# Kernel optimization log

Hardware: AMD Instinct MI355X
Metric: run time of the kernel (lower is better)

Reference implementation:

```python
import jax, jax.numpy as jnp
import numpy as np

H = 16
BN_EPS = 1e-12

def setup_inputs() -> dict:
    key = jax.random.key(0)
    ks = jax.random.split(key, 12)
    B, S, D = 2, 2048, 1024
    sc_in = 1.0 / np.sqrt(D)
    inp = {
        "hidden_states": jax.random.normal(ks[0], (B, S, D), jnp.float32),
        "attention_mask": jnp.zeros((B, 1, 1, S), jnp.float32),
        "Wq": jax.random.normal(ks[1], (D, D), jnp.float32) * sc_in,
        "bq": jnp.zeros((D,), jnp.float32),
        "Wk": jax.random.normal(ks[2], (D, D), jnp.float32) * sc_in,
        "bk": jnp.zeros((D,), jnp.float32),
        "Wv": jax.random.normal(ks[3], (D, D), jnp.float32) * sc_in,
        "bv": jnp.zeros((D,), jnp.float32),
        "pW1": jax.random.normal(ks[4], (D, 64), jnp.float32) * sc_in,
        "pb1": jnp.zeros((64,), jnp.float32),
        "bn_gamma": jnp.ones((64,), jnp.float32),
        "bn_beta": jnp.zeros((64,), jnp.float32),
        "bn_mean": jnp.zeros((64,), jnp.float32),
        "bn_var": jnp.ones((64,), jnp.float32),
        "pW2": jax.random.normal(ks[5], (64, H), jnp.float32) * (1.0 / 8.0),
        "pb2": jnp.zeros((H,), jnp.float32),
    }
    return inp


def reference(hidden_states, attention_mask, Wq, bq, Wk, bk, Wv, bv,
              pW1, pb1, bn_gamma, bn_beta, bn_mean, bn_var, pW2, pb2):
    B, S, D = hidden_states.shape
    hd = D // H
    scale = 1.0 / jnp.sqrt(jnp.asarray(hd, hidden_states.dtype))

    def split_heads(x):  # [B,S,D] -> [B,H,S,hd]
        return x.reshape(B, S, H, hd).transpose(0, 2, 1, 3)

    q = split_heads(hidden_states @ Wq + bq)
    k = split_heads(hidden_states @ Wk + bk)
    v = split_heads(hidden_states @ Wv + bv)

    scores = jnp.einsum("bhqd,bhkd->bhqk", q, k) * scale + attention_mask
    probs = jax.nn.softmax(scores, axis=-1)

    # head-gate predictor (layer_id == 0 -> mean pooling over sequence)
    pooled = jnp.mean(hidden_states, axis=1)  # [B,D]
    h = pooled @ pW1 + pb1
    h = (h - bn_mean) * jax.lax.rsqrt(bn_var + BN_EPS) * bn_gamma + bn_beta
    h = jax.nn.relu(h)
    logits = h @ pW2 + pb2  # [B,H]
    # inference-mode gumbel gate: hard threshold at 0
    head_gate = (logits >= 0).astype(probs.dtype)  # [B,H]

    probs = probs * head_gate[:, :, None, None]
    ctx = jnp.einsum("bhqk,bhkd->bhqd", probs, v)
    return ctx.transpose(0, 2, 1, 3).reshape(B, S, D)
```

## Files before the change

### kernel.cpp

```cpp
#include <hip/hip_runtime.h>

#define S_LEN 2048
#define D_DIM 1024
#define NH 16
#define HD 64
#define BATCH 2

#define QK_SCALE 0.18033688011112042f
#define LOG2E 1.4426950408889634f

using s16x8 = __attribute__((ext_vector_type(8))) short;
using u16x8 = __attribute__((ext_vector_type(8))) unsigned short;
using f32x4 = __attribute__((ext_vector_type(4))) float;
using bf16x8v = __attribute__((ext_vector_type(8))) __bf16;

typedef const __attribute__((address_space(1))) unsigned int* gas_ptr;
typedef __attribute__((address_space(3))) unsigned int* las_ptr;

__device__ __forceinline__ unsigned short f32_to_bf16(float f) {
  unsigned int u = __float_as_uint(f);
  u += 0x7FFFu + ((u >> 16) & 1u);
  return (unsigned short)(u >> 16);
}

__device__ __forceinline__ f32x4 mfma_bf16(s16x8 a, s16x8 b, f32x4 c) {
  return __builtin_amdgcn_mfma_f32_16x16x32_bf16(
      __builtin_bit_cast(bf16x8v, a), __builtin_bit_cast(bf16x8v, b), c, 0, 0, 0);
}

__device__ __forceinline__ float exp2_fast(float x) {
  float r;
  asm("v_exp_f32 %0, %1" : "=v"(r) : "v"(x));
  return r;
}

__device__ __forceinline__ unsigned int cvt_pk_bf16(float a, float b) {
  unsigned int r;
  asm("v_cvt_pk_bf16_f32 %0, %1, %2" : "=v"(r) : "v"(a), "v"(b));
  return r;
}

__global__ __launch_bounds__(256) void pool_cvt(const float* __restrict__ hs,
                                                unsigned short* __restrict__ hsb,
                                                float* __restrict__ partial) {
  int bid = blockIdx.x;
  int b = bid & 1;
  int chunk = (bid >> 1) & 31;
  int dq = bid >> 6;
  int d = dq * 256 + threadIdx.x;
  const float* p = hs + ((size_t)b * S_LEN + chunk * 64) * D_DIM + d;
  unsigned short* o = hsb + ((size_t)b * S_LEN + chunk * 64) * D_DIM + d;
  float s = 0.f;
  for (int i = 0; i < 64; ++i) {
    float v = p[(size_t)i * D_DIM];
    s += v;
    o[(size_t)i * D_DIM] = f32_to_bf16(v);
  }
  partial[(size_t)(b * 32 + chunk) * D_DIM + d] = s;
}

__global__ __launch_bounds__(256) void transpose_w3(
    const float* __restrict__ Wq, const float* __restrict__ Wk,
    const float* __restrict__ Wv, unsigned short* __restrict__ WTq,
    unsigned short* __restrict__ WTk, unsigned short* __restrict__ WTv) {
  __shared__ float tile[32][33];
  int z = blockIdx.z;
  const float* W = (z == 0) ? Wq : (z == 1) ? Wk : Wv;
  unsigned short* WT = (z == 0) ? WTq : (z == 1) ? WTk : WTv;
  float scale = (z == 0) ? QK_SCALE : 1.0f;
  int tx = threadIdx.x & 31;
  int ty = threadIdx.x >> 5;
  int c0 = blockIdx.x * 32;
  int r0 = blockIdx.y * 32;
#pragma unroll
  for (int i = 0; i < 4; ++i)
    tile[ty + i * 8][tx] = W[(r0 + ty + i * 8) * D_DIM + c0 + tx];
  __syncthreads();
#pragma unroll
  for (int i = 0; i < 4; ++i)
    WT[(c0 + ty + i * 8) * D_DIM + r0 + tx] = f32_to_bf16(tile[tx][ty + i * 8] * scale);
}

__global__ __launch_bounds__(512) void gate_kernel(
    const float* __restrict__ partial, const float* __restrict__ pW1,
    const float* __restrict__ pb1, const float* __restrict__ gamma,
    const float* __restrict__ beta, const float* __restrict__ mean,
    const float* __restrict__ var, const float* __restrict__ pW2,
    const float* __restrict__ pb2, float* __restrict__ gate) {
  __shared__ float pooled[2 * D_DIM];
  __shared__ float hsh[2][64];
  int t = threadIdx.x;
  for (int idx = t; idx < 2 * D_DIM; idx += 512) {
    int b = idx >> 10, k = idx & 1023;
    float s = 0.f;
#pragma unroll
    for (int c = 0; c < 32; ++c) s += partial[(size_t)(b * 32 + c) * D_DIM + k];
    pooled[idx] = s * (1.0f / 2048.0f);
  }
  __syncthreads();
  int b = t >> 8, jj = (t >> 2) & 63, quarter = t & 3;
  float acc = 0.f;
  for (int k = quarter * 256; k < quarter * 256 + 256; ++k)
    acc += pooled[b * D_DIM + k] * pW1[k * 64 + jj];
  acc += __shfl_xor(acc, 1, 64);
  acc += __shfl_xor(acc, 2, 64);
  if (quarter == 0) {
    acc += pb1[jj];
    acc = (acc - mean[jj]) * rsqrtf(var[jj] + 1e-12f) * gamma[jj] + beta[jj];
    hsh[b][jj] = fmaxf(acc, 0.f);
  }
  __syncthreads();
  if (t < 32) {
    int bb = t >> 4, hh = t & 15;
    float lg = pb2[hh];
#pragma unroll
    for (int kk = 0; kk < 64; ++kk) lg += hsh[bb][kk] * pW2[kk * NH + hh];
    gate[bb * NH + hh] = (lg >= 0.f) ? 1.f : 0.f;
  }
}

__global__ __launch_bounds__(256) void proj_gemm3(
    const unsigned short* __restrict__ A, const unsigned short* __restrict__ BT,
    const float* __restrict__ bq, const float* __restrict__ bk,
    const float* __restrict__ bv, unsigned short* __restrict__ Qb,
    unsigned short* __restrict__ Kb, unsigned short* __restrict__ Vtb) {
  __shared__ __align__(16) unsigned short As[128 * 64];
  __shared__ __align__(16) unsigned short Bs[128 * 64];
  int idx = blockIdx.x;
  int xcd = idx & 7, j = idx >> 3;
  int xm = xcd * 4 + j / 24;
  int yn = j % 24;
  int m0 = xm * 128, n0 = yn * 128;
  int tid = threadIdx.x, wave = tid >> 6, lane = tid & 63;
  int l15 = lane & 15, lhi = lane >> 4;
  int wm = (wave >> 1) * 64, wn = (wave & 1) * 64;
  f32x4 acc[4][4] = {};

  const unsigned short* asrc[4];
  const unsigned short* bsrc[4];
  int ldst[4];
#pragma unroll
  for (int r4 = 0; r4 < 4; ++r4) {
    int o = tid * 16 + r4 * 4096;
    int row = o >> 7;
    int e = ((o & 127) ^ ((row & 7) << 4)) >> 1;
    asrc[r4] = A + (size_t)(m0 + row) * D_DIM + e;
    bsrc[r4] = BT + (size_t)(n0 + row) * D_DIM + e;
    ldst[r4] = o >> 1;
  }
  int rsw = (l15 & 7) << 4;

  for (int k0 = 0; k0 < D_DIM; k0 += 64) {
#pragma unroll
    for (int r4 = 0; r4 < 4; ++r4) {
      __builtin_amdgcn_global_load_lds((gas_ptr)(asrc[r4] + k0),
                                       (las_ptr)(As + ldst[r4]), 16, 0, 0);
      __builtin_amdgcn_global_load_lds((gas_ptr)(bsrc[r4] + k0),
                                       (las_ptr)(Bs + ldst[r4]), 16, 0, 0);
    }
    __syncthreads();
    __builtin_amdgcn_s_setprio(1);
#pragma unroll
    for (int ks = 0; ks < 2; ++ks) {
      s16x8 af[4], bf[4];
#pragma unroll
      for (int mi = 0; mi < 4; ++mi)
        af[mi] = *(const s16x8*)((const char*)As + (wm + mi * 16 + l15) * 128 +
                                 ((ks * 64 + lhi * 16) ^ rsw));
#pragma unroll
      for (int ni = 0; ni < 4; ++ni)
        bf[ni] = *(const s16x8*)((const char*)Bs + (wn + ni * 16 + l15) * 128 +
                                 ((ks * 64 + lhi * 16) ^ rsw));
#pragma unroll
      for (int mi = 0; mi < 4; ++mi)
#pragma unroll
        for (int ni = 0; ni < 4; ++ni)
          acc[mi][ni] = mfma_bf16(af[mi], bf[ni], acc[mi][ni]);
    }
    __builtin_amdgcn_s_setprio(0);
    __syncthreads();
  }

#pragma unroll
  for (int mi = 0; mi < 4; ++mi)
#pragma unroll
    for (int ni = 0; ni < 4; ++ni) {
      int row0 = m0 + wm + mi * 16 + lhi * 4;
      int col = n0 + wn + ni * 16 + l15;
      int seg = col >> 10, c = col & 1023;
      if (seg == 2) {
        float bvv = bv[c];
        int h = c >> 6, d = c & 63;
        int b = row0 >> 11, s = row0 & 2047;
        ushort4 pk;
        pk.x = f32_to_bf16(acc[mi][ni][0] + bvv);
        pk.y = f32_to_bf16(acc[mi][ni][1] + bvv);
        pk.z = f32_to_bf16(acc[mi][ni][2] + bvv);
        pk.w = f32_to_bf16(acc[mi][ni][3] + bvv);
        *(ushort4*)&Vtb[((size_t)(b * NH + h) * HD + d) * S_LEN + s] = pk;
      } else {
        float bb2 = (seg == 0) ? bq[c] * QK_SCALE : bk[c];
        unsigned short* dst = (seg == 0) ? Qb : Kb;
        int h = c >> 6, d = c & 63;
#pragma unroll
        for (int r = 0; r < 4; ++r) {
          int row = row0 + r;
          int b = row >> 11, s = row & 2047;
          dst[((size_t)(b * NH + h) * S_LEN + s) * HD + d] =
              f32_to_bf16(acc[mi][ni][r] + bb2);
        }
      }
    }
}

__global__ __launch_bounds__(128) void attn_kernel(
    const unsigned short* __restrict__ Q, const unsigned short* __restrict__ K,
    const unsigned short* __restrict__ Vt, const float* __restrict__ mask,
    const float* __restrict__ gate, float* __restrict__ Out) {
  __shared__ __align__(16) unsigned short Ks[2][4096];
  __shared__ __align__(16) unsigned short Vs[2][4096];
  __shared__ __align__(16) unsigned short p_lds[2][2][1024];

  int idx = blockIdx.x;
  int xcd = idx & 7;
  int slot = idx >> 3;
  int qc = slot & 31;
  int r = (slot >> 5) * 8 + xcd;
  int tid = threadIdx.x;
  int wave = tid >> 6, lane = tid & 63;
  int l15 = lane & 15, lhi = lane >> 4;

  float gv = (lane < 32) ? gate[lane] : 0.f;
  unsigned long long live = __ballot(gv != 0.f);
  int W = __popcll(live);
  bool working = (r < W);
  int want = working ? r : (r - W);
  unsigned long long M = working ? live : (~live & 0xFFFFFFFFull);
  int head = 0, c = 0;
#pragma unroll
  for (int hh = 0; hh < 32; ++hh) {
    if ((M >> hh) & 1) {
      if (c == want) head = hh;
      ++c;
    }
  }
  int b = head >> 4, h = head & 15;

  if (!working) {
    float4 z = {0.f, 0.f, 0.f, 0.f};
    int row = qc * 64 + (tid >> 1);
    float* op = Out + ((size_t)b * S_LEN + row) * D_DIM + h * HD + (tid & 1) * 32;
#pragma unroll
    for (int dd = 0; dd < 8; ++dd) *(float4*)(op + dd * 4) = z;
    return;
  }

  int qA = qc * 64 + wave * 32 + l15;
  int qB = qA + 16;
  const unsigned short* Qp = Q + (size_t)head * S_LEN * HD;
  const unsigned short* Kp = K + (size_t)head * S_LEN * HD;
  const unsigned short* Vp = Vt + (size_t)head * HD * S_LEN;
  const float* maskp = mask + (size_t)b * S_LEN;

  int psw = (l15 & 7) << 4;
  const unsigned short* kb[4];
  const unsigned short* vb[4];
  int ldst[4];
#pragma unroll
  for (int j = 0; j < 4; ++j) {
    int o = tid * 16 + j * 2048;
    int row = o >> 7, col = o & 127;
    int e = (col ^ ((row & 7) << 4)) >> 1;
    kb[j] = Kp + row * HD + e;
    vb[j] = Vp + (size_t)row * S_LEN + e;
    ldst[j] = o >> 1;
  }

#define STAGE(BUFI, KTV)                                                           \
  {                                                                                \
    _Pragma("unroll") for (int j = 0; j < 4; ++j) {                                \
      __builtin_amdgcn_global_load_lds((gas_ptr)(kb[j] + (size_t)(KTV)*HD),        \
                                       (las_ptr)(&Ks[BUFI][ldst[j]]), 16, 0, 0);   \
      __builtin_amdgcn_global_load_lds((gas_ptr)(vb[j] + (KTV)),                   \
                                       (las_ptr)(&Vs[BUFI][ldst[j]]), 16, 0, 0);   \
    }                                                                              \
  }

  STAGE(0, 0);
  float4 mvc[4];
#pragma unroll
  for (int nf = 0; nf < 4; ++nf)
    mvc[nf] = *(const float4*)(maskp + nf * 16 + lhi * 4);

  s16x8 qfa[2], qfb[2];
#pragma unroll
  for (int ks = 0; ks < 2; ++ks) {
    qfa[ks] = *(const s16x8*)(Qp + (size_t)qA * HD + ks * 32 + lhi * 8);
    qfb[ks] = *(const s16x8*)(Qp + (size_t)qB * HD + ks * 32 + lhi * 8);
  }

  int swz0 = (lhi * 16) ^ psw;
  int swz1 = (64 + lhi * 16) ^ psw;
  char* pbaseA = (char*)p_lds + wave * 4096 + l15 * 128;
  char* pbaseB = pbaseA + 2048;

  f32x4 oa[4] = {}, ob[4] = {};
  float sa_run = 0.f, sb_run = 0.f;

  __syncthreads();

  for (int kt = 0; kt < S_LEN; kt += 64) {
    int buf = (kt >> 6) & 1;
    int ktn = (kt + 64) & (S_LEN - 1);
    STAGE(buf ^ 1, ktn);
    float4 mvn[4];
#pragma unroll
    for (int nf = 0; nf < 4; ++nf)
      mvn[nf] = *(const float4*)(maskp + ktn + nf * 16 + lhi * 4);

    const char* kc = (const char*)&Ks[0][0] + buf * 8192;
    f32x4 sa[4] = {}, sb[4] = {};
    __builtin_amdgcn_s_setprio(1);
#pragma unroll
    for (int nf = 0; nf < 4; ++nf) {
      int rb = (nf * 16 + l15) * 128;
      s16x8 a0 = *(const s16x8*)(kc + (rb + swz0));
      s16x8 a1 = *(const s16x8*)(kc + (rb + swz1));
      sa[nf] = mfma_bf16(a0, qfa[0], sa[nf]);
      sa[nf] = mfma_bf16(a1, qfa[1], sa[nf]);
      sb[nf] = mfma_bf16(a0, qfb[0], sb[nf]);
      sb[nf] = mfma_bf16(a1, qfb[1], sb[nf]);
    }
    __builtin_amdgcn_s_setprio(0);

    float psa[4], psb[4];
#pragma unroll
    for (int nf = 0; nf < 4; ++nf) {
#pragma unroll
      for (int rr = 0; rr < 4; ++rr) {
        float m2 = ((const float*)&mvc[nf])[rr] * LOG2E;
        sa[nf][rr] = exp2_fast(sa[nf][rr] + m2);
        sb[nf][rr] = exp2_fast(sb[nf][rr] + m2);
      }
      psa[nf] = (sa[nf][0] + sa[nf][1]) + (sa[nf][2] + sa[nf][3]);
      psb[nf] = (sb[nf][0] + sb[nf][1]) + (sb[nf][2] + sb[nf][3]);
    }
    sa_run += (psa[0] + psa[1]) + (psa[2] + psa[3]);
    sb_run += (psb[0] + psb[1]) + (psb[2] + psb[3]);

#pragma unroll
    for (int nf = 0; nf < 4; ++nf) {
      uint2 pka, pkb;
      pka.x = cvt_pk_bf16(sa[nf][0], sa[nf][1]);
      pka.y = cvt_pk_bf16(sa[nf][2], sa[nf][3]);
      pkb.x = cvt_pk_bf16(sb[nf][0], sb[nf][1]);
      pkb.y = cvt_pk_bf16(sb[nf][2], sb[nf][3]);
      int off = (nf * 32 + lhi * 8) ^ psw;
      *(uint2*)(pbaseA + off) = pka;
      *(uint2*)(pbaseB + off) = pkb;
    }

    const char* vc = (const char*)&Vs[0][0] + buf * 8192;
    __builtin_amdgcn_s_setprio(1);
#pragma unroll
    for (int ks = 0; ks < 2; ++ks) {
      int sw = ks ? swz1 : swz0;
      int poff = (ks * 64 + lhi * 16) ^ psw;
      s16x8 pfa = *(const s16x8*)(pbaseA + poff);
      s16x8 pfb = *(const s16x8*)(pbaseB + poff);
#pragma unroll
      for (int df = 0; df < 4; ++df) {
        s16x8 vf = *(const s16x8*)(vc + ((df * 16 + l15) * 128 + sw));
        oa[df] = mfma_bf16(vf, pfa, oa[df]);
        ob[df] = mfma_bf16(vf, pfb, ob[df]);
      }
    }
    __builtin_amdgcn_s_setprio(0);

    __syncthreads();
#pragma unroll
    for (int nf = 0; nf < 4; ++nf) mvc[nf] = mvn[nf];
  }
#undef STAGE

  float sa_tot = sa_run, sb_tot = sb_run;
  sa_tot += __shfl_xor(sa_tot, 16, 64);
  sa_tot += __shfl_xor(sa_tot, 32, 64);
  sb_tot += __shfl_xor(sb_tot, 16, 64);
  sb_tot += __shfl_xor(sb_tot, 32, 64);
  float inva = 1.0f / sa_tot;
  float invb = 1.0f / sb_tot;

#pragma unroll
  for (int df = 0; df < 4; ++df) {
    float4 ova, ovb;
    ova.x = oa[df][0] * inva; ova.y = oa[df][1] * inva;
    ova.z = oa[df][2] * inva; ova.w = oa[df][3] * inva;
    ovb.x = ob[df][0] * invb; ovb.y = ob[df][1] * invb;
    ovb.z = ob[df][2] * invb; ovb.w = ob[df][3] * invb;
    *(float4*)(Out + ((size_t)b * S_LEN + qA) * D_DIM + h * HD + df * 16 + lhi * 4) = ova;
    *(float4*)(Out + ((size_t)b * S_LEN + qB) * D_DIM + h * HD + df * 16 + lhi * 4) = ovb;
  }
}


extern "C" void kernel_launch(void* const* d_in, const int* in_sizes, int n_in,
                              void* d_out, int out_size, void* d_ws, size_t ws_size,
                              hipStream_t stream) {
  (void)in_sizes; (void)n_in; (void)out_size; (void)ws_size;
  const float* hs   = (const float*)d_in[0];
  const float* mask = (const float*)d_in[1];
  const float* Wq   = (const float*)d_in[2];
  const float* bq   = (const float*)d_in[3];
  const float* Wk   = (const float*)d_in[4];
  const float* bk   = (const float*)d_in[5];
  const float* Wv   = (const float*)d_in[6];
  const float* bv   = (const float*)d_in[7];
  const float* pW1  = (const float*)d_in[8];
  const float* pb1  = (const float*)d_in[9];
  const float* gam  = (const float*)d_in[10];
  const float* bet  = (const float*)d_in[11];
  const float* mea  = (const float*)d_in[12];
  const float* var  = (const float*)d_in[13];
  const float* pW2  = (const float*)d_in[14];
  const float* pb2  = (const float*)d_in[15];
  float* out = (float*)d_out;

  const size_t MB = 1u << 20;
  char* ws = (char*)d_ws;
  unsigned short* hsb = (unsigned short*)(ws);
  unsigned short* wTq = (unsigned short*)(ws + 8 * MB);
  unsigned short* wTk = (unsigned short*)(ws + 10 * MB);
  unsigned short* wTv = (unsigned short*)(ws + 12 * MB);
  unsigned short* Qb  = (unsigned short*)(ws + 14 * MB);
  unsigned short* Kb  = (unsigned short*)(ws + 22 * MB);
  unsigned short* Vtb = (unsigned short*)(ws + 30 * MB);
  float* partial = (float*)(ws + 38 * MB);
  float* gateb   = (float*)(ws + 38 * MB + 262144);

  pool_cvt<<<256, 256, 0, stream>>>(hs, hsb, partial);
  transpose_w3<<<dim3(32, 32, 3), 256, 0, stream>>>(Wq, Wk, Wv, wTq, wTk, wTv);
  gate_kernel<<<1, 512, 0, stream>>>(partial, pW1, pb1, gam, bet, mea, var, pW2, pb2, gateb);

  proj_gemm3<<<768, 256, 0, stream>>>(hsb, wTq, bq, bk, bv, Qb, Kb, Vtb);

  attn_kernel<<<1024, 128, 0, stream>>>(Qb, Kb, Vtb, mask, gateb, out);
}
```

Before: 135.7 us.

## Use single-wave attention blocks and replace barriers with vmcnt waits

```diff
diff --git a/kernel.cpp b/kernel.cpp
--- a/kernel.cpp
+++ b/kernel.cpp
@@ -213,21 +213,20 @@
     }
 }
 
-__global__ __launch_bounds__(128) void attn_kernel(
+__global__ __launch_bounds__(64) void attn_kernel(
     const unsigned short* __restrict__ Q, const unsigned short* __restrict__ K,
     const unsigned short* __restrict__ Vt, const float* __restrict__ mask,
     const float* __restrict__ gate, float* __restrict__ Out) {
   __shared__ __align__(16) unsigned short Ks[2][4096];
   __shared__ __align__(16) unsigned short Vs[2][4096];
-  __shared__ __align__(16) unsigned short p_lds[2][2][1024];
+  __shared__ __align__(16) unsigned short p_lds[2][1024];
 
   int idx = blockIdx.x;
   int xcd = idx & 7;
   int slot = idx >> 3;
-  int qc = slot & 31;
-  int r = (slot >> 5) * 8 + xcd;
-  int tid = threadIdx.x;
-  int wave = tid >> 6, lane = tid & 63;
+  int qc = slot & 63;
+  int r = (slot >> 6) * 8 + xcd;
+  int lane = threadIdx.x;
   int l15 = lane & 15, lhi = lane >> 4;
 
   float gv = (lane < 32) ? gate[lane] : 0.f;
@@ -248,14 +247,14 @@
 
   if (!working) {
     float4 z = {0.f, 0.f, 0.f, 0.f};
-    int row = qc * 64 + (tid >> 1);
-    float* op = Out + ((size_t)b * S_LEN + row) * D_DIM + h * HD + (tid & 1) * 32;
+    int row = qc * 32 + (lane >> 1);
+    float* op = Out + ((size_t)b * S_LEN + row) * D_DIM + h * HD + (lane & 1) * 32;
 #pragma unroll
     for (int dd = 0; dd < 8; ++dd) *(float4*)(op + dd * 4) = z;
     return;
   }
 
-  int qA = qc * 64 + wave * 32 + l15;
+  int qA = qc * 32 + l15;
   int qB = qA + 16;
   const unsigned short* Qp = Q + (size_t)head * S_LEN * HD;
   const unsigned short* Kp = K + (size_t)head * S_LEN * HD;
@@ -263,27 +262,21 @@
   const float* maskp = mask + (size_t)b * S_LEN;
 
   int psw = (l15 & 7) << 4;
-  const unsigned short* kb[4];
-  const unsigned short* vb[4];
-  int ldst[4];
-#pragma unroll
-  for (int j = 0; j < 4; ++j) {
-    int o = tid * 16 + j * 2048;
-    int row = o >> 7, col = o & 127;
-    int e = (col ^ ((row & 7) << 4)) >> 1;
-    kb[j] = Kp + row * HD + e;
-    vb[j] = Vp + (size_t)row * S_LEN + e;
-    ldst[j] = o >> 1;
-  }
+  int e = (((lane & 7) * 16) ^ ((lane >> 3) << 4)) >> 1;
+  const unsigned short* kbase = Kp + (size_t)(lane >> 3) * HD + e;
+  const unsigned short* vbase = Vp + (size_t)(lane >> 3) * S_LEN + e;
+  int l0 = lane * 8;
 
 #define STAGE(BUFI, KTV)                                                           \
   {                                                                                \
-    _Pragma("unroll") for (int j = 0; j < 4; ++j) {                                \
-      __builtin_amdgcn_global_load_lds((gas_ptr)(kb[j] + (size_t)(KTV)*HD),        \
-                                       (las_ptr)(&Ks[BUFI][ldst[j]]), 16, 0, 0);   \
-      __builtin_amdgcn_global_load_lds((gas_ptr)(vb[j] + (KTV)),                   \
-                                       (las_ptr)(&Vs[BUFI][ldst[j]]), 16, 0, 0);   \
-    }                                                                              \
+    _Pragma("unroll") for (int j = 0; j < 8; ++j)                                  \
+        __builtin_amdgcn_global_load_lds(                                          \
+            (gas_ptr)(kbase + (size_t)(KTV) * HD + j * 8 * HD),                    \
+            (las_ptr)(&Ks[BUFI][l0 + j * 512]), 16, 0, 0);                         \
+    _Pragma("unroll") for (int j = 0; j < 8; ++j)                                  \
+        __builtin_amdgcn_global_load_lds(                                          \
+            (gas_ptr)(vbase + (KTV) + (size_t)j * 8 * S_LEN),                      \
+            (las_ptr)(&Vs[BUFI][l0 + j * 512]), 16, 0, 0);                         \
   }
 
   STAGE(0, 0);
@@ -301,13 +294,11 @@
 
   int swz0 = (lhi * 16) ^ psw;
   int swz1 = (64 + lhi * 16) ^ psw;
-  char* pbaseA = (char*)p_lds + wave * 4096 + l15 * 128;
+  char* pbaseA = (char*)p_lds + l15 * 128;
   char* pbaseB = pbaseA + 2048;
 
   f32x4 oa[4] = {}, ob[4] = {};
   float sa_run = 0.f, sb_run = 0.f;
-
-  __syncthreads();
 
   for (int kt = 0; kt < S_LEN; kt += 64) {
     int buf = (kt >> 6) & 1;
@@ -317,6 +308,8 @@
 #pragma unroll
     for (int nf = 0; nf < 4; ++nf)
       mvn[nf] = *(const float4*)(maskp + ktn + nf * 16 + lhi * 4);
+
+    asm volatile("s_waitcnt vmcnt(20)" ::: "memory");
 
     const char* kc = (const char*)&Ks[0][0] + buf * 8192;
     f32x4 sa[4] = {}, sb[4] = {};
@@ -333,7 +326,6 @@
     }
     __builtin_amdgcn_s_setprio(0);
 
-    float psa[4], psb[4];
 #pragma unroll
     for (int nf = 0; nf < 4; ++nf) {
 #pragma unroll
@@ -342,11 +334,9 @@
         sa[nf][rr] = exp2_fast(sa[nf][rr] + m2);
         sb[nf][rr] = exp2_fast(sb[nf][rr] + m2);
       }
-      psa[nf] = (sa[nf][0] + sa[nf][1]) + (sa[nf][2] + sa[nf][3]);
-      psb[nf] = (sb[nf][0] + sb[nf][1]) + (sb[nf][2] + sb[nf][3]);
-    }
-    sa_run += (psa[0] + psa[1]) + (psa[2] + psa[3]);
-    sb_run += (psb[0] + psb[1]) + (psb[2] + psb[3]);
+      sa_run += (sa[nf][0] + sa[nf][1]) + (sa[nf][2] + sa[nf][3]);
+      sb_run += (sb[nf][0] + sb[nf][1]) + (sb[nf][2] + sb[nf][3]);
+    }
 
 #pragma unroll
     for (int nf = 0; nf < 4; ++nf) {
@@ -377,7 +367,6 @@
     }
     __builtin_amdgcn_s_setprio(0);
 
-    __syncthreads();
 #pragma unroll
     for (int nf = 0; nf < 4; ++nf) mvc[nf] = mvn[nf];
   }
@@ -444,5 +433,5 @@
 
   proj_gemm3<<<768, 256, 0, stream>>>(hsb, wTq, bq, bk, bv, Qb, Kb, Vtb);
 
-  attn_kernel<<<1024, 128, 0, stream>>>(Qb, Kb, Vtb, mask, gateb, out);
-}
+  attn_kernel<<<2048, 64, 0, stream>>>(Qb, Kb, Vtb, mask, gateb, out);
+}
```

New measurement: 172.8 us. 27.4% more time.
